# Optimization experiments

Hardware: AMD Instinct MI355X
Metric: run time of the kernel (lower is better)

Reference implementation:

```python
import jax, jax.numpy as jnp
import numpy as np

SEQ, D_MODEL, N_HEADS, D_INT = 2048, 1024, 16, 64
D_OUT = D_MODEL // N_HEADS  # 64


def setup_inputs() -> dict:
    key = jax.random.key(0)
    ks = jax.random.split(key, 9)
    s = lambda fan_in: 1.0 / np.sqrt(fan_in)
    return {
        "input_vecs": jax.random.normal(ks[0], (8, SEQ, D_MODEL), dtype=jnp.float32),
        # weights stored [in, out] (torch Linear weight transposed)
        "Wk": jax.random.uniform(ks[1], (D_MODEL, D_INT), minval=-s(D_MODEL), maxval=s(D_MODEL)),
        "bk": jax.random.uniform(ks[2], (D_INT,), minval=-s(D_MODEL), maxval=s(D_MODEL)),
        "Wq": jax.random.uniform(ks[3], (D_MODEL, D_INT), minval=-s(D_MODEL), maxval=s(D_MODEL)),
        "bq": jax.random.uniform(ks[4], (D_INT,), minval=-s(D_MODEL), maxval=s(D_MODEL)),
        "Wv": jax.random.uniform(ks[5], (D_MODEL, D_INT), minval=-s(D_MODEL), maxval=s(D_MODEL)),
        "bv": jax.random.uniform(ks[6], (D_INT,), minval=-s(D_MODEL), maxval=s(D_MODEL)),
        "W0": jax.random.uniform(ks[7], (D_INT, D_OUT), minval=-s(D_INT), maxval=s(D_INT)),
        "b0": jax.random.uniform(ks[8], (D_OUT,), minval=-s(D_INT), maxval=s(D_INT)),
    }


def reference(input_vecs, Wk, bk, Wq, bq, Wv, bv, W0, b0):
    # Projections: [B, T, d_int]
    k = jnp.einsum("btd,de->bte", input_vecs, Wk) + bk
    q = jnp.einsum("btd,de->bte", input_vecs, Wq) + bq
    v = jnp.einsum("btd,de->bte", input_vecs, Wv) + bv
    d_k = k.shape[-1]
    # Causal scores: [B, T, T]
    scores = jnp.einsum("bqe,bke->bqk", q, k) * (d_k ** -0.5)
    T = scores.shape[-1]
    causal = jnp.tril(jnp.ones((T, T), dtype=bool))
    scores = jnp.where(causal, scores, -jnp.inf)
    attn = jax.nn.softmax(scores, axis=-1)
    ctx = jnp.einsum("bqk,bke->bqe", attn, v)  # [B, T, d_int]
    return jnp.einsum("bte,eo->bto", ctx, W0) + b0  # [B, T, d_model//num_heads]
```

## Files before the change

### kernel.cpp

```cpp
#include <hip/hip_runtime.h>
#include <math.h>

#define SEQ 2048
#define DM  1024
#define DI  64

typedef __attribute__((ext_vector_type(8))) short short8;
typedef __attribute__((ext_vector_type(4))) float f32x4;
typedef __attribute__((ext_vector_type(4))) unsigned short ush4;

#define MFMA16(a,b,c) __builtin_amdgcn_mfma_f32_16x16x32_bf16(a,b,c,0,0,0)

__device__ __forceinline__ unsigned short f2bf(float f) {
    unsigned int u = __builtin_bit_cast(unsigned int, f);
    u += 0x7fffu + ((u >> 16) & 1u);
    return (unsigned short)(u >> 16);
}


__global__ __launch_bounds__(256)
void convert_kernel(const float* __restrict__ Wq, const float* __restrict__ Wk,
                    const float* __restrict__ Wv, const float* __restrict__ W0,
                    const float* __restrict__ bq, const float* __restrict__ bk,
                    const float* __restrict__ bv,
                    unsigned short* __restrict__ Wf, unsigned short* __restrict__ W0f,
                    float* __restrict__ bcat)
{
    const int t = threadIdx.x;
    const int blk = blockIdx.x;
    if (blk < 96) {
        const int flat = blk * 256 + t;
        const int lane = flat & 63;
        const int s    = (flat >> 6) & 1;
        const int gk   = flat >> 7;
        const int g = gk >> 4, ks = gk & 15;
        const int n = lane & 15, quad = lane >> 4;
        const int ocat = 16 * g + n;
        const int mat = ocat >> 6, o = ocat & 63;
        const float* src = (mat == 0) ? Wq : (mat == 1) ? Wk : Wv;
        const float scale = (mat == 0) ? 0.125f : 1.0f;
        const int kb = ks * 64 + s * 32 + quad * 8;
        union { short8 v; unsigned short u[8]; } pk;
#pragma unroll
        for (int e = 0; e < 8; ++e)
            pk.u[e] = f2bf(src[(size_t)(kb + e) * DI + o] * scale);
        *(short8*)(Wf + (size_t)flat * 8) = pk.v;
    } else {
        const int flat = (blk - 96) * 256 + t;
        if (flat < 512) {
            const int lane = flat & 63;
            const int s    = (flat >> 6) & 1;
            const int g    = flat >> 7;
            const int n = lane & 15, quad = lane >> 4;
            const int o = 16 * g + n;
            const int kb = s * 32 + quad * 8;
            union { short8 v; unsigned short u[8]; } pk;
#pragma unroll
            for (int e = 0; e < 8; ++e)
                pk.u[e] = f2bf(W0[(size_t)(kb + e) * DI + o]);
            *(short8*)(W0f + (size_t)flat * 8) = pk.v;
        }
        if (blk == 96 && t < 192)
            bcat[t] = (t < 64) ? bq[t] * 0.125f : (t < 128) ? bk[t - 64] : bv[t - 128];
    }
}

__global__ __launch_bounds__(256, 2)
void proj_kernel(const float* __restrict__ X, const unsigned short* __restrict__ Wf,
                 const float* __restrict__ bcat,
                 unsigned short* __restrict__ Qf, unsigned short* __restrict__ Kf,
                 unsigned short* __restrict__ Vf)
{
    __shared__ alignas(16) unsigned short Xs[32 * 1024];
    const int t = threadIdx.x;
    const int lane = t & 63, w = t >> 6;
    const int quad = lane >> 4, n = lane & 15;
    const int r0 = blockIdx.x * 32;

    {
        const int r = t >> 4, g = t & 15;
        const int s = g >> 3, qd = (g >> 1) & 3, e0 = (g & 1) * 4;
        const int base = (r * 4 + qd) * 8 + e0;
#pragma unroll
        for (int th = 0; th < 2; ++th) {
            const float* xp = X + (size_t)(r0 + th * 16 + r) * DM + g * 4;
#pragma unroll
            for (int i = 0; i < 16; ++i) {
                const float4 x = *(const float4*)(xp + i * 64);
                union { ush4 v; unsigned short u[4]; } px;
                px.u[0] = f2bf(x.x); px.u[1] = f2bf(x.y);
                px.u[2] = f2bf(x.z); px.u[3] = f2bf(x.w);
                *(ush4*)(Xs + th * 16384 + (i * 2 + s) * 512 + base) = px.v;
            }
        }
    }
    __syncthreads();

    const unsigned short* wb0 = Wf + (size_t)(3 * w + 0) * 16384 + lane * 8;
    const unsigned short* wb1 = Wf + (size_t)(3 * w + 1) * 16384 + lane * 8;
    const unsigned short* wb2 = Wf + (size_t)(3 * w + 2) * 16384 + lane * 8;
    const int aperm = (n * 4 + quad) * 8;

    const f32x4 ZERO = {0.f, 0.f, 0.f, 0.f};
    f32x4 acc[2][3];
#pragma unroll
    for (int th = 0; th < 2; ++th)
#pragma unroll
        for (int j = 0; j < 3; ++j) acc[th][j] = ZERO;

#pragma unroll 2
    for (int ks = 0; ks < 16; ++ks) {
        short8 af[2][2], bf[3][2];
#pragma unroll
        for (int s = 0; s < 2; ++s) {
            const size_t o = (size_t)(ks * 2 + s) * 512;
            af[0][s] = *(const short8*)(Xs + o + aperm);
            af[1][s] = *(const short8*)(Xs + 16384 + o + aperm);
            bf[0][s] = *(const short8*)(wb0 + o);
            bf[1][s] = *(const short8*)(wb1 + o);
            bf[2][s] = *(const short8*)(wb2 + o);
        }
#pragma unroll
        for (int th = 0; th < 2; ++th)
#pragma unroll
            for (int j = 0; j < 3; ++j) {
                acc[th][j] = MFMA16(af[th][0], bf[j][0], acc[th][j]);
                acc[th][j] = MFMA16(af[th][1], bf[j][1], acc[th][j]);
            }
    }

    __syncthreads();
    unsigned short (*Facc)[200] = (unsigned short (*)[200])Xs;
    float bias[3];
#pragma unroll
    for (int j = 0; j < 3; ++j) bias[j] = bcat[(3 * w + j) * 16 + n];
#pragma unroll
    for (int th = 0; th < 2; ++th)
#pragma unroll
        for (int j = 0; j < 3; ++j)
#pragma unroll
            for (int r = 0; r < 4; ++r)
                Facc[th * 16 + quad * 4 + r][(3 * w + j) * 16 + n] = f2bf(acc[th][j][r] + bias[j]);
    __syncthreads();

    const int bidx = r0 >> 11;
    const int qt16 = (r0 >> 4) & 127;
    const int kc   = (r0 >> 6) & 31;
    const int sblk = (r0 >> 5) & 1;
    {
        const int qsel = t >> 7, s = (t >> 6) & 1, lp = t & 63;
        const int np = lp & 15, qp = lp >> 4;
        const int row = qsel * 16 + np, col = s * 32 + qp * 8;
        const size_t off = (size_t)(((bidx * 128 + qt16 + qsel) * 2 + s) * 64 + lp) * 8;
        *(short8*)(Qf + off) = *(const short8*)&Facc[row][col];
        *(short8*)(Kf + off) = *(const short8*)&Facc[row][64 + col];
    }
    {
        const int nt = t >> 6, lp = t & 63;
        const int np = lp & 15, qp = lp >> 4;
        union { short8 v; unsigned short u[8]; } ov;
#pragma unroll
        for (int e = 0; e < 8; ++e) ov.u[e] = Facc[qp * 8 + e][128 + 16 * nt + np];
        const size_t off = (size_t)((((bidx * 4 + nt) * 32 + kc) * 2 + sblk) * 64 + lp) * 8;
        *(short8*)(Vf + off) = ov.v;
    }
}

__global__ __launch_bounds__(256, 2)
void attn_kernel(const unsigned short* __restrict__ Qf, const unsigned short* __restrict__ Kf,
                 const unsigned short* __restrict__ Vf, const unsigned short* __restrict__ W0f,
                 const float* __restrict__ b0, float* __restrict__ Out)
{
    __shared__ alignas(16) float pool[4][32][72];
    __shared__ alignas(16) unsigned short Cb[32][72];
    __shared__ float Lp[4][32][4];

    const int t = threadIdx.x;
    const int lane = t & 63, w = t >> 6;
    const int quad = lane >> 4, n = lane & 15;
    const int qt = 63 - (blockIdx.x >> 3);
    const int b  = blockIdx.x & 7;
    const int q0 = qt * 32;

    unsigned short* P0 = (unsigned short*)&pool[w][0][0];
    unsigned short* P1 = P0 + 32 * 72;

    short8 qf[2][2];
#pragma unroll
    for (int qh = 0; qh < 2; ++qh)
#pragma unroll
        for (int s = 0; s < 2; ++s)
            qf[qh][s] = *(const short8*)(Qf + (size_t)(((b*128 + qt*2 + qh)*2 + s)*64 + lane) * 8);

    const f32x4 ZERO = {0.f, 0.f, 0.f, 0.f};
    f32x4 ctx[2][4];
#pragma unroll
    for (int qh = 0; qh < 2; ++qh)
#pragma unroll
        for (int nt = 0; nt < 4; ++nt) ctx[qh][nt] = ZERO;
    float rs[2] = {0.f, 0.f};
    const float M0 = 8.0f;

    const int C = (qt >> 1) + 1;

#define DO_CHUNK(KT, PB, KFX, VFX)                                             \
    do {                                                                       \
        const int k0_ = (KT) * 64;                                             \
        f32x4 sv[2][4];                                                        \
        _Pragma("unroll")                                                      \
        for (int qh = 0; qh < 2; ++qh)                                         \
            _Pragma("unroll")                                                  \
            for (int tt = 0; tt < 4; ++tt) {                                   \
                f32x4 a_ = MFMA16(KFX[tt][0], qf[qh][0], ZERO);                \
                sv[qh][tt] = MFMA16(KFX[tt][1], qf[qh][1], a_);                \
            }                                                                  \
        if ((KT) == C - 1) {                                                   \
            _Pragma("unroll")                                                  \
            for (int qh = 0; qh < 2; ++qh)                                     \
                _Pragma("unroll")                                              \
                for (int tt = 0; tt < 4; ++tt)                                 \
                    _Pragma("unroll")                                          \
                    for (int r = 0; r < 4; ++r)                                \
                        if (k0_ + 16*tt + quad*4 + r > q0 + qh*16 + n)         \
                            sv[qh][tt][r] = -INFINITY;                         \
        }                                                                      \
        _Pragma("unroll")                                                      \
        for (int qh = 0; qh < 2; ++qh)                                         \
            _Pragma("unroll")                                                  \
            for (int tt = 0; tt < 4; ++tt) {                                   \
                union { ush4 v; unsigned short u[4]; } pw;                     \
                _Pragma("unroll")                                              \
                for (int r = 0; r < 4; ++r) {                                  \
                    const float p_ = __expf(sv[qh][tt][r] - M0);               \
                    rs[qh] += p_;                                              \
                    pw.u[r] = f2bf(p_);                                        \
                }                                                              \
                *(ush4*)&(PB)[(size_t)(qh*16 + n) * 72 + 16*tt + quad*4] = pw.v; \
            }                                                                  \
        _Pragma("unroll")                                                      \
        for (int s = 0; s < 2; ++s) {                                          \
            const short8 pf0 = *(const short8*)&(PB)[(size_t)(n)      * 72 + s*32 + quad*8]; \
            const short8 pf1 = *(const short8*)&(PB)[(size_t)(16 + n) * 72 + s*32 + quad*8]; \
            _Pragma("unroll")                                                  \
            for (int nt = 0; nt < 4; ++nt) {                                   \
                ctx[0][nt] = MFMA16(pf0, VFX[nt][s], ctx[0][nt]);              \
                ctx[1][nt] = MFMA16(pf1, VFX[nt][s], ctx[1][nt]);              \
            }                                                                  \
        }                                                                      \
    } while (0)

    short8 kfA[4][2], vfA[4][2];
    if (w < C) {
#pragma unroll
        for (int tt = 0; tt < 4; ++tt)
#pragma unroll
            for (int s = 0; s < 2; ++s) {
                kfA[tt][s] = *(const short8*)(Kf + (size_t)(((b*128 + w*4 + tt)*2 + s)*64 + lane) * 8);
                vfA[tt][s] = *(const short8*)(Vf + (size_t)((((b*4 + tt)*32 + w)*2 + s)*64 + lane) * 8);
            }
    }
    for (int kt0 = w; kt0 < C; kt0 += 8) {
        const int ktB = kt0 + 4;
        const bool hasB = (ktB < C);
        short8 kfB[4][2];
        if (hasB) {
#pragma unroll
            for (int tt = 0; tt < 4; ++tt)
#pragma unroll
                for (int s = 0; s < 2; ++s)
                    kfB[tt][s] = *(const short8*)(Kf + (size_t)(((b*128 + ktB*4 + tt)*2 + s)*64 + lane) * 8);
        }
        DO_CHUNK(kt0, P0, kfA, vfA);
        const int ktN = kt0 + 8;
        const bool hasN = (ktN < C);
        short8 kfN[4][2], vfN[4][2];
        if (hasN) {
#pragma unroll
            for (int tt = 0; tt < 4; ++tt)
#pragma unroll
                for (int s = 0; s < 2; ++s) {
                    kfN[tt][s] = *(const short8*)(Kf + (size_t)(((b*128 + ktN*4 + tt)*2 + s)*64 + lane) * 8);
                    vfN[tt][s] = *(const short8*)(Vf + (size_t)((((b*4 + tt)*32 + ktN)*2 + s)*64 + lane) * 8);
                }
        }
        if (hasB) {
            short8 vfB[4][2];
#pragma unroll
            for (int tt = 0; tt < 4; ++tt)
#pragma unroll
                for (int s = 0; s < 2; ++s)
                    vfB[tt][s] = *(const short8*)(Vf + (size_t)((((b*4 + tt)*32 + ktB)*2 + s)*64 + lane) * 8);
            DO_CHUNK(ktB, P1, kfB, vfB);
        }
        if (hasN) {
#pragma unroll
            for (int tt = 0; tt < 4; ++tt)
#pragma unroll
                for (int s = 0; s < 2; ++s) {
                    kfA[tt][s] = kfN[tt][s];
                    vfA[tt][s] = vfN[tt][s];
                }
        }
    }
#undef DO_CHUNK

#pragma unroll
    for (int qh = 0; qh < 2; ++qh) {
#pragma unroll
        for (int nt = 0; nt < 4; ++nt)
#pragma unroll
            for (int r = 0; r < 4; ++r)
                pool[w][qh*16 + quad*4 + r][nt*16 + n] = ctx[qh][nt][r];
        Lp[w][qh*16 + n][quad] = rs[qh];
    }
    __syncthreads();

    {
        const int q = t >> 3, c0 = (t & 7) * 8;
        float l = 0.f;
#pragma unroll
        for (int w4 = 0; w4 < 4; ++w4)
#pragma unroll
            for (int qd = 0; qd < 4; ++qd) l += Lp[w4][q][qd];
        const float inv = 1.0f / l;
        float s[8];
#pragma unroll
        for (int j = 0; j < 8; ++j) s[j] = 0.f;
#pragma unroll
        for (int w4 = 0; w4 < 4; ++w4) {
            const float4 a = *(const float4*)&pool[w4][q][c0];
            const float4 c = *(const float4*)&pool[w4][q][c0 + 4];
            s[0] += a.x; s[1] += a.y; s[2] += a.z; s[3] += a.w;
            s[4] += c.x; s[5] += c.y; s[6] += c.z; s[7] += c.w;
        }
        union { short8 v; unsigned short u[8]; } cb;
#pragma unroll
        for (int j = 0; j < 8; ++j) cb.u[j] = f2bf(s[j] * inv);
        *(short8*)&Cb[q][c0] = cb.v;
    }
    __syncthreads();

    f32x4 oacc[2] = {ZERO, ZERO};
#pragma unroll
    for (int s = 0; s < 2; ++s) {
        const short8 wf = *(const short8*)(W0f + (size_t)((w*2 + s)*64 + lane) * 8);
#pragma unroll
        for (int tt = 0; tt < 2; ++tt) {
            const short8 cf = *(const short8*)&Cb[tt*16 + n][s*32 + quad*8];
            oacc[tt] = MFMA16(cf, wf, oacc[tt]);
        }
    }
    const float bb = b0[16*w + n];
#pragma unroll
    for (int tt = 0; tt < 2; ++tt)
#pragma unroll
        for (int r = 0; r < 4; ++r)
            Out[((size_t)b * SEQ + q0 + tt*16 + quad*4 + r) * DI + 16*w + n] = oacc[tt][r] + bb;
}

extern "C" void kernel_launch(void* const* d_in, const int* in_sizes, int n_in,
                              void* d_out, int out_size, void* d_ws, size_t ws_size,
                              hipStream_t stream) {
    const float* X  = (const float*)d_in[0];
    const float* Wk = (const float*)d_in[1];
    const float* bk = (const float*)d_in[2];
    const float* Wq = (const float*)d_in[3];
    const float* bq = (const float*)d_in[4];
    const float* Wv = (const float*)d_in[5];
    const float* bv = (const float*)d_in[6];
    const float* W0 = (const float*)d_in[7];
    const float* b0 = (const float*)d_in[8];
    float* Out = (float*)d_out;

    unsigned char* ws = (unsigned char*)d_ws;
    unsigned short* Wf   = (unsigned short*)ws;
    unsigned short* W0f  = (unsigned short*)(ws + 393216);
    float*          bcat = (float*)(ws + 401408);
    unsigned short* Qf   = (unsigned short*)(ws + 409600);
    unsigned short* Kf   = (unsigned short*)(ws + 409600 + 2097152);
    unsigned short* Vf   = (unsigned short*)(ws + 409600 + 4194304);

    convert_kernel<<<98, 256, 0, stream>>>(Wq, Wk, Wv, W0, bq, bk, bv, Wf, W0f, bcat);
    proj_kernel<<<512, 256, 0, stream>>>(X, Wf, bcat, Qf, Kf, Vf);
    attn_kernel<<<512, 256, 0, stream>>>(Qf, Kf, Vf, W0f, b0, Out);
}
```

Baseline: 128.7 us.

## Use packed bf16 converts, exp2 softmax with folded log2e, and balanced block order

Replaces the software float-to-bf16 rounding with the hardware v_cvt_pk_bf16_f32 packed convert in the projection, softmax and context stages. It folds log2(e) into the Q scale so the softmax can use a native exp2 instead of __expf. It splits the row-sum accumulation into two chains to shorten the dependency. It also reorders attention blocks so the heavy late query tiles are interleaved with light early ones, to balance causal work across CUs. The main risk is small numeric differences from the different rounding path and the folded constant.

```diff
diff --git a/kernel.cpp b/kernel.cpp
--- a/kernel.cpp
+++ b/kernel.cpp
@@ -16,6 +16,23 @@
     u += 0x7fffu + ((u >> 16) & 1u);
     return (unsigned short)(u >> 16);
 }
+
+__device__ __forceinline__ unsigned int cvtpk(float lo, float hi) {
+    unsigned int r;
+    asm("v_cvt_pk_bf16_f32 %0, %1, %2" : "=v"(r) : "v"(lo), "v"(hi));
+    return r;
+}
+
+__device__ __forceinline__ float exp2_fast(float x) {
+#if __has_builtin(__builtin_amdgcn_exp2f)
+    return __builtin_amdgcn_exp2f(x);
+#else
+    return exp2f(x);
+#endif
+}
+
+#define QSCALE 0.18033688011112042f
+#define M0L2   11.541560327111707f
 
 
 __global__ __launch_bounds__(256)
@@ -38,7 +55,7 @@
         const int ocat = 16 * g + n;
         const int mat = ocat >> 6, o = ocat & 63;
         const float* src = (mat == 0) ? Wq : (mat == 1) ? Wk : Wv;
-        const float scale = (mat == 0) ? 0.125f : 1.0f;
+        const float scale = (mat == 0) ? QSCALE : 1.0f;
         const int kb = ks * 64 + s * 32 + quad * 8;
         union { short8 v; unsigned short u[8]; } pk;
 #pragma unroll
@@ -61,7 +78,7 @@
             *(short8*)(W0f + (size_t)flat * 8) = pk.v;
         }
         if (blk == 96 && t < 192)
-            bcat[t] = (t < 64) ? bq[t] * 0.125f : (t < 128) ? bk[t - 64] : bv[t - 128];
+            bcat[t] = (t < 64) ? bq[t] * QSCALE : (t < 128) ? bk[t - 64] : bv[t - 128];
     }
 }
 
@@ -87,9 +104,9 @@
 #pragma unroll
             for (int i = 0; i < 16; ++i) {
                 const float4 x = *(const float4*)(xp + i * 64);
-                union { ush4 v; unsigned short u[4]; } px;
-                px.u[0] = f2bf(x.x); px.u[1] = f2bf(x.y);
-                px.u[2] = f2bf(x.z); px.u[3] = f2bf(x.w);
+                union { unsigned int wd[2]; ush4 v; } px;
+                px.wd[0] = cvtpk(x.x, x.y);
+                px.wd[1] = cvtpk(x.z, x.w);
                 *(ush4*)(Xs + th * 16384 + (i * 2 + s) * 512 + base) = px.v;
             }
         }
@@ -178,7 +195,8 @@
     const int t = threadIdx.x;
     const int lane = t & 63, w = t >> 6;
     const int quad = lane >> 4, n = lane & 15;
-    const int qt = 63 - (blockIdx.x >> 3);
+    const int g  = blockIdx.x >> 3;
+    const int qt = (g < 32) ? (63 - g) : (g - 32);
     const int b  = blockIdx.x & 7;
     const int q0 = qt * 32;
 
@@ -198,8 +216,7 @@
     for (int qh = 0; qh < 2; ++qh)
 #pragma unroll
         for (int nt = 0; nt < 4; ++nt) ctx[qh][nt] = ZERO;
-    float rs[2] = {0.f, 0.f};
-    const float M0 = 8.0f;
+    float rs2[2][2] = {{0.f, 0.f}, {0.f, 0.f}};
 
     const int C = (qt >> 1) + 1;
 
@@ -228,13 +245,15 @@
         for (int qh = 0; qh < 2; ++qh)                                         \
             _Pragma("unroll")                                                  \
             for (int tt = 0; tt < 4; ++tt) {                                   \
-                union { ush4 v; unsigned short u[4]; } pw;                     \
+                float p_[4];                                                   \
                 _Pragma("unroll")                                              \
                 for (int r = 0; r < 4; ++r) {                                  \
-                    const float p_ = __expf(sv[qh][tt][r] - M0);               \
-                    rs[qh] += p_;                                              \
-                    pw.u[r] = f2bf(p_);                                        \
+                    p_[r] = exp2_fast(sv[qh][tt][r] - M0L2);                   \
+                    rs2[qh][r & 1] += p_[r];                                   \
                 }                                                              \
+                union { unsigned int wd[2]; ush4 v; } pw;                      \
+                pw.wd[0] = cvtpk(p_[0], p_[1]);                                \
+                pw.wd[1] = cvtpk(p_[2], p_[3]);                                \
                 *(ush4*)&(PB)[(size_t)(qh*16 + n) * 72 + 16*tt + quad*4] = pw.v; \
             }                                                                  \
         _Pragma("unroll")                                                      \
@@ -311,7 +330,7 @@
 #pragma unroll
             for (int r = 0; r < 4; ++r)
                 pool[w][qh*16 + quad*4 + r][nt*16 + n] = ctx[qh][nt][r];
-        Lp[w][qh*16 + n][quad] = rs[qh];
+        Lp[w][qh*16 + n][quad] = rs2[qh][0] + rs2[qh][1];
     }
     __syncthreads();
 
@@ -333,9 +352,10 @@
             s[0] += a.x; s[1] += a.y; s[2] += a.z; s[3] += a.w;
             s[4] += c.x; s[5] += c.y; s[6] += c.z; s[7] += c.w;
         }
-        union { short8 v; unsigned short u[8]; } cb;
-#pragma unroll
-        for (int j = 0; j < 8; ++j) cb.u[j] = f2bf(s[j] * inv);
+        union { unsigned int wd[4]; short8 v; } cb;
+#pragma unroll
+        for (int j = 0; j < 4; ++j)
+            cb.wd[j] = cvtpk(s[2*j] * inv, s[2*j + 1] * inv);
         *(short8*)&Cb[q][c0] = cb.v;
     }
     __syncthreads();
```

Result: faster. 125.6 us, median of 2 (-2.4%).
